# Optimization experiments

Measured on AMD Instinct MI355X. Metric: run time of the kernel, lower is better.

## Reference

```python
import jax, jax.numpy as jnp
import numpy as np

SHARPNESS = 1000.0   # sigmoid temperature from source: *1000.0
BIAS = 0.008         # shadow acne bias from source: -0.008
FILTER_SIZE = 1      # 3x3 PCF
SHADOW_STEP = 1


def setup_inputs() -> dict:
    key = jax.random.key(0)
    k1, k2, k3 = jax.random.split(key, 3)
    N, H, W, K, S = 8, 1024, 1024, 1, 2048
    # light-view depth buffer (fragments_from_light.zbuf), K=1 squeezed
    light_zbuf = jax.random.uniform(k1, (N, S, S), dtype=jnp.float32)
    depth_z = jax.random.uniform(k2, (N, H, W, K), dtype=jnp.float32)
    # rounded integer light-screen coords per camera pixel: [..., 0]=x, [..., 1]=y
    xy = jax.random.randint(k3, (N, H, W, K, 2), 0, S, dtype=jnp.int32)
    return {"light_zbuf": light_zbuf, "depth_z": depth_z, "xy": xy, "image_size": S}


def reference(light_zbuf, depth_z, xy, image_size):
    N, H, W, K = depth_z.shape
    b = jnp.arange(N, dtype=jnp.int32)[:, None, None, None]  # broadcast batch index
    x = xy[..., 0]  # [N,H,W,K]
    y = xy[..., 1]
    aa = depth_z - BIAS
    vis = jnp.zeros_like(depth_z)
    # 3x3 PCF: gather clamped neighbors in the light zbuf, soft depth test, accumulate
    for ii in range(-FILTER_SIZE, FILTER_SIZE + 1):
        for jj in range(-FILTER_SIZE, FILTER_SIZE + 1):
            yi = jnp.clip(y + ii * SHADOW_STEP, 0, image_size - 1)
            xi = jnp.clip(x + jj * SHADOW_STEP, 0, image_size - 1)
            bb = light_zbuf[b, yi, xi]  # [N,H,W,K] gather
            vis = vis + jax.nn.sigmoid((bb - aa) * SHARPNESS)
    return vis / float((1 + 2 * FILTER_SIZE) ** 2)
```

## Files before the change

### kernel.cpp

```cpp
#include <hip/hip_runtime.h>


#define SHARPNESS 1000.0f
#define BIAS 0.008f
#define S2LOG2E 1442.6950408889634f

#define S_IMG     2048
#define NBATCH    8
#define HWK       (1 << 20)
#define TSH       6
#define TPS       (S_IMG >> TSH)
#define BPB       (TPS * TPS)
#define NBINS     (NBATCH * BPB)
#define SLAB_CAP  1280
#define STW       66
#define REC_BYTES ((size_t)NBINS * SLAB_CAP * 4ull)
#define WS_NEED   (REC_BYTES + (size_t)NBINS * 4ull)

#define P1_BLOCKS 512
#define PXB       16384

typedef int i4v __attribute__((ext_vector_type(4)));

__device__ __forceinline__ float sigf(float bb, float a) {
    const float t = (a - bb) * S2LOG2E;
    return __builtin_amdgcn_rcpf(1.0f + exp2f(t));
}

__global__ __launch_bounds__(1024, 8) void p1_bin(
    const int* __restrict__ xy_raw,
    unsigned* __restrict__ recs, unsigned* __restrict__ gcur)
{
    __shared__ unsigned cnt[BPB];
    __shared__ unsigned cur[BPB];
    const int blk   = blockIdx.x;
    const int tid   = threadIdx.x;
    const int batch = blk >> 6;
    const int ilb   = (blk & 63) * PXB;
    if (tid < BPB) cnt[tid] = 0;
    __syncthreads();

    unsigned pk[16];
    const i4v* xy4 = (const i4v*)xy_raw + (size_t)blk * (PXB / 2);
#pragma unroll
    for (int j = 0; j < 8; ++j) {
        const i4v q = __builtin_nontemporal_load(&xy4[j * 1024 + tid]);
        pk[2 * j]     = (unsigned)q.x | ((unsigned)q.y << 11);
        pk[2 * j + 1] = (unsigned)q.z | ((unsigned)q.w << 11);
        atomicAdd(&cnt[((q.y >> TSH) << 5) | (q.x >> TSH)], 1u);
        atomicAdd(&cnt[((q.w >> TSH) << 5) | (q.z >> TSH)], 1u);
    }
    __syncthreads();

    if (tid < BPB) cur[tid] = atomicAdd(&gcur[batch * BPB + tid], cnt[tid]);
    __syncthreads();

#pragma unroll
    for (int j = 0; j < 16; ++j) {
        const int x  = (int)(pk[j] & 0x7FFu);
        const int y  = (int)(pk[j] >> 11);
        const int bn = ((y >> TSH) << 5) | (x >> TSH);
        const unsigned pos = atomicAdd(&cur[bn], 1u);
        const int il = ilb + 2 * ((j >> 1) * 1024 + tid) + (j & 1);
        const unsigned rec = (unsigned)il
                           | ((unsigned)(x & 63) << 20)
                           | ((unsigned)(y & 63) << 26);
        if (pos < SLAB_CAP)
            recs[(size_t)(batch * BPB + bn) * SLAB_CAP + pos] = rec;
    }
}

__global__ __launch_bounds__(256, 8) void p2_pcf(
    const float* __restrict__ zbuf, const float* __restrict__ depth,
    const unsigned* __restrict__ recs, const unsigned* __restrict__ gcur,
    float* __restrict__ out)
{
    __shared__ float zt[STW * STW];
    const int bin   = blockIdx.x;
    const int batch = bin >> 10;
    const int t     = bin & (BPB - 1);
    const int tx    = t & (TPS - 1);
    const int ty    = t >> 5;
    const int tid   = threadIdx.x;
    const float* zb = zbuf + (size_t)batch * ((size_t)S_IMG * S_IMG);
    const int x0 = tx * 64 - 1, y0 = ty * 64 - 1;

    for (int i = tid; i < STW * STW; i += 256) {
        const int r  = i / STW;
        const int c  = i - r * STW;
        const int gy = min(max(y0 + r, 0), S_IMG - 1);
        const int gx = min(max(x0 + c, 0), S_IMG - 1);
        zt[i] = zb[(size_t)gy * S_IMG + gx];
    }
    __syncthreads();

    const int n = min((int)gcur[bin], SLAB_CAP);
    const unsigned* slab = recs + (size_t)bin * SLAB_CAP;
    const float* dpb = depth + (size_t)batch * HWK;
    float*       opb = out + (size_t)batch * HWK;

    for (int k = tid; k < n; k += 256) {
        const unsigned rec = __builtin_nontemporal_load(&slab[k]);
        const int il = (int)(rec & 0xFFFFFu);
        const int xl = (int)((rec >> 20) & 63u);
        const int yl = (int)(rec >> 26);
        const float a = dpb[il] - BIAS;
        const float* p = zt + yl * STW + xl;
        const float vis =
              sigf(p[0],           a) + sigf(p[1],           a) + sigf(p[2],           a)
            + sigf(p[STW],         a) + sigf(p[STW + 1],     a) + sigf(p[STW + 2],     a)
            + sigf(p[2 * STW],     a) + sigf(p[2 * STW + 1], a) + sigf(p[2 * STW + 2], a);
        opb[il] = vis * (1.0f / 9.0f);
    }
}

__global__ __launch_bounds__(256) void pcf_shadow_generic(
    const float* __restrict__ zbuf, const float* __restrict__ depth_z,
    const int2* __restrict__ xy, const int* __restrict__ image_size_p,
    float* __restrict__ out, int total, int zbuf_elems)
{
    const int i = blockIdx.x * blockDim.x + threadIdx.x;
    if (i >= total) return;
    const int S  = *image_size_p;
    const int SS = S * S;
    const int N  = zbuf_elems / SS;
    const int hwk = total / N;
    const int b   = i / hwk;
    const float a = depth_z[i] - BIAS;
    const int2 p  = xy[i];
    const float* base = zbuf + (size_t)b * (size_t)SS;
    float vis = 0.0f;
#pragma unroll
    for (int ii = -1; ii <= 1; ++ii) {
        const int yi = min(max(p.y + ii, 0), S - 1);
        const float* row = base + (size_t)yi * (size_t)S;
#pragma unroll
        for (int jj = -1; jj <= 1; ++jj) {
            const int xi = min(max(p.x + jj, 0), S - 1);
            vis += 1.0f / (1.0f + __expf((a - row[xi]) * SHARPNESS));
        }
    }
    out[i] = vis * (1.0f / 9.0f);
}

extern "C" void kernel_launch(void* const* d_in, const int* in_sizes, int n_in,
                              void* d_out, int out_size, void* d_ws, size_t ws_size,
                              hipStream_t stream) {
    const float* zbuf     = (const float*)d_in[0];
    const float* depth_z  = (const float*)d_in[1];
    const int*   xy_raw   = (const int*)d_in[2];
    const int*   img_size = (const int*)d_in[3];
    float*       out      = (float*)d_out;

    const int zbuf_elems = in_sizes[0];
    const int total      = in_sizes[1];

    if (zbuf_elems == NBATCH * S_IMG * S_IMG && total == NBATCH * HWK &&
        ws_size >= WS_NEED) {
        unsigned* recs = (unsigned*)d_ws;
        unsigned* gcur = (unsigned*)((char*)d_ws + REC_BYTES);
        hipMemsetAsync(gcur, 0, (size_t)NBINS * 4ull, stream);
        p1_bin<<<P1_BLOCKS, 1024, 0, stream>>>(xy_raw, recs, gcur);
        p2_pcf<<<NBINS, 256, 0, stream>>>(zbuf, depth_z, recs, gcur, out);
    } else {
        const int block = 256;
        const int grid  = (total + block - 1) / block;
        pcf_shadow_generic<<<grid, block, 0, stream>>>(zbuf, depth_z, (const int2*)xy_raw,
                                                       img_size, out, total, zbuf_elems);
    }
}
```

Measured before the change: 492.1 us.

## Carry depth in bin records and add coalesced output scatter pass

Binning now stores each pixel's depth with its tile-local coordinates, and records a per-pixel slot index. The tile kernel reads depth straight from the slab, so it no longer gathers depth randomly, and it writes the PCF result back into the slab. A third kernel then reads the slot indices in pixel order and writes the output with coalesced stores. Pixels that overflow a bin are now computed directly rather than dropped, so the result stays correct beyond the cap. The trade is an extra pass, larger 8-byte records and an index array, all meant to replace random 4-byte depth reads and output writes with streaming accesses.

```diff
diff --git a/kernel.cpp b/kernel.cpp
--- a/kernel.cpp
+++ b/kernel.cpp
@@ -5,113 +5,179 @@
 #define BIAS 0.008f
 #define S2LOG2E 1442.6950408889634f
 
-#define S_IMG     2048
-#define NBATCH    8
-#define HWK       (1 << 20)
-#define TSH       6
-#define TPS       (S_IMG >> TSH)
-#define BPB       (TPS * TPS)
-#define NBINS     (NBATCH * BPB)
-#define SLAB_CAP  1280
-#define STW       66
-#define REC_BYTES ((size_t)NBINS * SLAB_CAP * 4ull)
-#define WS_NEED   (REC_BYTES + (size_t)NBINS * 4ull)
-
-#define P1_BLOCKS 512
-#define PXB       16384
-
-typedef int i4v __attribute__((ext_vector_type(4)));
+#define S_IMG   2048
+#define NBATCH  8
+#define HWK     (1 << 20)
+#define TSH     6
+#define TPS     32
+#define BPB     (TPS * TPS)
+#define CAP     1280
+#define STW     66
+#define PXB     16384
+#define SENT    0xFFFFFFFFu
+
+typedef int      i4v __attribute__((ext_vector_type(4)));
+typedef float    f2v __attribute__((ext_vector_type(2)));
+typedef float    f4v __attribute__((ext_vector_type(4)));
+typedef unsigned u2v __attribute__((ext_vector_type(2)));
 
 __device__ __forceinline__ float sigf(float bb, float a) {
     const float t = (a - bb) * S2LOG2E;
     return __builtin_amdgcn_rcpf(1.0f + exp2f(t));
 }
 
-__global__ __launch_bounds__(1024, 8) void p1_bin(
-    const int* __restrict__ xy_raw,
-    unsigned* __restrict__ recs, unsigned* __restrict__ gcur)
+__global__ __launch_bounds__(1024, 2) void p1_bin(
+    const int* __restrict__ xy_raw, const float* __restrict__ depth,
+    u2v* __restrict__ slab, unsigned* __restrict__ pidx,
+    unsigned* __restrict__ gcur, int b0)
 {
     __shared__ unsigned cnt[BPB];
     __shared__ unsigned cur[BPB];
-    const int blk   = blockIdx.x;
-    const int tid   = threadIdx.x;
-    const int batch = blk >> 6;
-    const int ilb   = (blk & 63) * PXB;
-    if (tid < BPB) cnt[tid] = 0;
-    __syncthreads();
-
-    unsigned pk[16];
-    const i4v* xy4 = (const i4v*)xy_raw + (size_t)blk * (PXB / 2);
+    const int blk = blockIdx.x;
+    const int bl  = blk >> 6;
+    const int sub = blk & 63;
+    const int tid = threadIdx.x;
+    cnt[tid] = 0;
+    __syncthreads();
+
+    const size_t pb_g = ((size_t)(b0 + bl)) * HWK + (size_t)sub * PXB;
+    const i4v* xq = (const i4v*)xy_raw + pb_g / 2;
+    const f2v* dq = (const f2v*)depth  + pb_g / 2;
+
+    unsigned pk[16]; float dd[16];
 #pragma unroll
     for (int j = 0; j < 8; ++j) {
-        const i4v q = __builtin_nontemporal_load(&xy4[j * 1024 + tid]);
+        const i4v q = __builtin_nontemporal_load(&xq[j * 1024 + tid]);
+        const f2v d = __builtin_nontemporal_load(&dq[j * 1024 + tid]);
         pk[2 * j]     = (unsigned)q.x | ((unsigned)q.y << 11);
         pk[2 * j + 1] = (unsigned)q.z | ((unsigned)q.w << 11);
+        dd[2 * j] = d.x; dd[2 * j + 1] = d.y;
         atomicAdd(&cnt[((q.y >> TSH) << 5) | (q.x >> TSH)], 1u);
         atomicAdd(&cnt[((q.w >> TSH) << 5) | (q.z >> TSH)], 1u);
     }
     __syncthreads();
-
-    if (tid < BPB) cur[tid] = atomicAdd(&gcur[batch * BPB + tid], cnt[tid]);
-    __syncthreads();
-
-#pragma unroll
-    for (int j = 0; j < 16; ++j) {
-        const int x  = (int)(pk[j] & 0x7FFu);
-        const int y  = (int)(pk[j] >> 11);
-        const int bn = ((y >> TSH) << 5) | (x >> TSH);
-        const unsigned pos = atomicAdd(&cur[bn], 1u);
-        const int il = ilb + 2 * ((j >> 1) * 1024 + tid) + (j & 1);
-        const unsigned rec = (unsigned)il
-                           | ((unsigned)(x & 63) << 20)
-                           | ((unsigned)(y & 63) << 26);
-        if (pos < SLAB_CAP)
-            recs[(size_t)(batch * BPB + bn) * SLAB_CAP + pos] = rec;
-    }
-}
-
-__global__ __launch_bounds__(256, 8) void p2_pcf(
-    const float* __restrict__ zbuf, const float* __restrict__ depth,
-    const unsigned* __restrict__ recs, const unsigned* __restrict__ gcur,
-    float* __restrict__ out)
+    cur[tid] = atomicAdd(&gcur[bl * BPB + tid], cnt[tid]);
+    __syncthreads();
+
+    const size_t pb_l = (size_t)bl * HWK + (size_t)sub * PXB;
+    u2v* px2 = (u2v*)pidx + pb_l / 2;
+#pragma unroll
+    for (int j = 0; j < 8; ++j) {
+        u2v pi;
+#pragma unroll
+        for (int e = 0; e < 2; ++e) {
+            const unsigned w = pk[2 * j + e];
+            const int x = (int)(w & 0x7FFu), y = (int)(w >> 11);
+            const int bn = ((y >> TSH) << 5) | (x >> TSH);
+            const unsigned pos = atomicAdd(&cur[bn], 1u);
+            unsigned v = SENT;
+            if (pos < CAP) {
+                const unsigned slot = (unsigned)(bl * BPB + bn) * CAP + pos;
+                u2v r;
+                r.x = (unsigned)(x & 63) | ((unsigned)(y & 63) << 6);
+                r.y = __float_as_uint(dd[2 * j + e]);
+                slab[slot] = r;
+                v = slot;
+            }
+            if (e == 0) pi.x = v; else pi.y = v;
+        }
+        px2[j * 1024 + tid] = pi;
+    }
+}
+
+__global__ __launch_bounds__(256, 8) void p2_tile(
+    const float* __restrict__ zbuf, u2v* __restrict__ slab,
+    const unsigned* __restrict__ gcur, int b0)
 {
     __shared__ float zt[STW * STW];
-    const int bin   = blockIdx.x;
-    const int batch = bin >> 10;
-    const int t     = bin & (BPB - 1);
-    const int tx    = t & (TPS - 1);
-    const int ty    = t >> 5;
-    const int tid   = threadIdx.x;
-    const float* zb = zbuf + (size_t)batch * ((size_t)S_IMG * S_IMG);
+    const int gb  = blockIdx.x;
+    const int tid = threadIdx.x;
+    const int bl  = gb >> 10;
+    const int t   = gb & (BPB - 1);
+    const int tx  = t & 31, ty = t >> 5;
+    const float* zb = zbuf + (size_t)(b0 + bl) * ((size_t)S_IMG * S_IMG);
     const int x0 = tx * 64 - 1, y0 = ty * 64 - 1;
 
+    const int n   = min((int)gcur[gb], CAP);
+    const int nc  = n - 1;
+    const int ncc = max(nc, 0);
+    u2v* sl = slab + (size_t)gb * CAP;
+
+    u2v Rc[5];
+#pragma unroll
+    for (int j = 0; j < 5; ++j)
+        Rc[j] = sl[min(j * 256 + tid, ncc)];
+
     for (int i = tid; i < STW * STW; i += 256) {
-        const int r  = i / STW;
-        const int c  = i - r * STW;
+        const int r  = i / STW, c = i - r * STW;
         const int gy = min(max(y0 + r, 0), S_IMG - 1);
         const int gx = min(max(x0 + c, 0), S_IMG - 1);
         zt[i] = zb[(size_t)gy * S_IMG + gx];
     }
     __syncthreads();
 
-    const int n = min((int)gcur[bin], SLAB_CAP);
-    const unsigned* slab = recs + (size_t)bin * SLAB_CAP;
-    const float* dpb = depth + (size_t)batch * HWK;
-    float*       opb = out + (size_t)batch * HWK;
-
-    for (int k = tid; k < n; k += 256) {
-        const unsigned rec = __builtin_nontemporal_load(&slab[k]);
-        const int il = (int)(rec & 0xFFFFFu);
-        const int xl = (int)((rec >> 20) & 63u);
-        const int yl = (int)(rec >> 26);
-        const float a = dpb[il] - BIAS;
-        const float* p = zt + yl * STW + xl;
+    float* slf = (float*)sl;
+#pragma unroll
+    for (int j = 0; j < 5; ++j) {
+        const unsigned w = Rc[j].x;
+        const float a  = __uint_as_float(Rc[j].y) - BIAS;
+        const float* p = zt + (int)((w >> 6) & 63u) * STW + (int)(w & 63u);
         const float vis =
               sigf(p[0],           a) + sigf(p[1],           a) + sigf(p[2],           a)
             + sigf(p[STW],         a) + sigf(p[STW + 1],     a) + sigf(p[STW + 2],     a)
             + sigf(p[2 * STW],     a) + sigf(p[2 * STW + 1], a) + sigf(p[2 * STW + 2], a);
-        opb[il] = vis * (1.0f / 9.0f);
-    }
+        const int k = j * 256 + tid;
+        if (k <= nc) slf[2 * k + 1] = vis * (1.0f / 9.0f);
+    }
+}
+
+__global__ __launch_bounds__(256) void p3_out(
+    const unsigned* __restrict__ pidx, const float* __restrict__ slabf,
+    float* __restrict__ out,
+    const float* __restrict__ zbuf, const float* __restrict__ depth,
+    const int* __restrict__ xy_raw, int b0)
+{
+    const int tid = threadIdx.x;
+    const i4v* px4 = (const i4v*)pidx;
+    const size_t gbase = (size_t)blockIdx.x * 1024;
+
+    i4v P[4];
+#pragma unroll
+    for (int j = 0; j < 4; ++j)
+        P[j] = __builtin_nontemporal_load(&px4[gbase + j * 256 + tid]);
+
+    f4v V[4];
+#pragma unroll
+    for (int j = 0; j < 4; ++j) {
+#pragma unroll
+        for (int e = 0; e < 4; ++e) {
+            const unsigned pi = (unsigned)P[j][e];
+            float v;
+            if (pi != SENT) {
+                v = slabf[2 * (size_t)pi + 1];
+            } else {
+                const size_t il = (size_t)b0 * HWK + (gbase + j * 256 + tid) * 4 + e;
+                const int batch = (int)(il >> 20);
+                const float a = depth[il] - BIAS;
+                const int x = xy_raw[2 * il], y = xy_raw[2 * il + 1];
+                const float* zbb = zbuf + (size_t)batch * ((size_t)S_IMG * S_IMG);
+                float vv = 0.0f;
+                for (int ii = -1; ii <= 1; ++ii) {
+                    const int yi = min(max(y + ii, 0), S_IMG - 1);
+                    const float* row = zbb + (size_t)yi * S_IMG;
+                    for (int jj = -1; jj <= 1; ++jj)
+                        vv += sigf(row[min(max(x + jj, 0), S_IMG - 1)], a);
+                }
+                v = vv * (1.0f / 9.0f);
+            }
+            V[j][e] = v;
+        }
+    }
+
+    f4v* o4 = (f4v*)(out + (size_t)b0 * HWK);
+#pragma unroll
+    for (int j = 0; j < 4; ++j)
+        __builtin_nontemporal_store(V[j], &o4[gbase + j * 256 + tid]);
 }
 
 __global__ __launch_bounds__(256) void pcf_shadow_generic(
@@ -155,17 +221,33 @@
     const int zbuf_elems = in_sizes[0];
     const int total      = in_sizes[1];
 
-    if (zbuf_elems == NBATCH * S_IMG * S_IMG && total == NBATCH * HWK &&
-        ws_size >= WS_NEED) {
-        unsigned* recs = (unsigned*)d_ws;
-        unsigned* gcur = (unsigned*)((char*)d_ws + REC_BYTES);
-        hipMemsetAsync(gcur, 0, (size_t)NBINS * 4ull, stream);
-        p1_bin<<<P1_BLOCKS, 1024, 0, stream>>>(xy_raw, recs, gcur);
-        p2_pcf<<<NBINS, 256, 0, stream>>>(zbuf, depth_z, recs, gcur, out);
-    } else {
-        const int block = 256;
-        const int grid  = (total + block - 1) / block;
-        pcf_shadow_generic<<<grid, block, 0, stream>>>(zbuf, depth_z, (const int2*)xy_raw,
-                                                       img_size, out, total, zbuf_elems);
-    }
-}
+    if (zbuf_elems == NBATCH * S_IMG * S_IMG && total == NBATCH * HWK) {
+        const size_t per_b = (size_t)BPB * CAP * 8ull + (size_t)HWK * 4ull
+                           + (size_t)BPB * 4ull;
+        int nb = 0;
+        if      (ws_size >= 8 * per_b) nb = 8;
+        else if (ws_size >= 4 * per_b) nb = 4;
+        else if (ws_size >= 2 * per_b) nb = 2;
+        else if (ws_size >= 1 * per_b) nb = 1;
+
+        if (nb) {
+            const size_t slab_b = (size_t)nb * BPB * CAP * 8ull;
+            const size_t pidx_b = (size_t)nb * HWK * 4ull;
+            u2v*      slab = (u2v*)d_ws;
+            unsigned* pidx = (unsigned*)((char*)d_ws + slab_b);
+            unsigned* gcur = (unsigned*)((char*)d_ws + slab_b + pidx_b);
+            for (int b0 = 0; b0 < NBATCH; b0 += nb) {
+                hipMemsetAsync(gcur, 0, (size_t)nb * BPB * 4ull, stream);
+                p1_bin<<<nb * 64,  1024, 0, stream>>>(xy_raw, depth_z, slab, pidx, gcur, b0);
+                p2_tile<<<nb * BPB, 256, 0, stream>>>(zbuf, slab, gcur, b0);
+                p3_out<<<nb * 256,  256, 0, stream>>>(pidx, (const float*)slab, out,
+                                                      zbuf, depth_z, xy_raw, b0);
+            }
+            return;
+        }
+    }
+    const int block = 256;
+    const int grid  = (total + block - 1) / block;
+    pcf_shadow_generic<<<grid, block, 0, stream>>>(zbuf, depth_z, (const int2*)xy_raw,
+                                                   img_size, out, total, zbuf_elems);
+}
```

After: 432.8 us. 1.14x faster.
